# Performance work log

Hardware: AMD Instinct MI355X
Metric: run time of the kernel (lower is better)

The kernel has to match this reference:

```python
import jax, jax.numpy as jnp
import numpy as np

N = 4096

def setup_inputs() -> dict:
    key = jax.random.key(0)
    kA, kB = jax.random.split(key)
    A = jnp.tril(jax.random.normal(kA, (N, N), dtype=jnp.float32))
    B = jnp.tril(jax.random.normal(kB, (N, N), dtype=jnp.float32))
    return {"A": A, "B": B}

def reference(A, B):
    # Product of two lower-triangular matrices; result is lower-triangular.
    # tril applied to the dense matmul reproduces the intended math exactly
    # (and zeroes any numerical noise in the structural-zero upper triangle).
    return jnp.tril(jnp.matmul(A, B))
```

## Files before the change

kernel.cpp:

```cpp
#include <hip/hip_runtime.h>
#include <stdint.h>

#define NN 4096
#define NB 32
#define BK 32

#define NHEAVY 136
#define NHUNITS 272
#define NLIGHT 392
#define ZBASE 664
#define TGRID 1160

#define PGRID 8328

typedef __bf16 bf16x8 __attribute__((ext_vector_type(8)));
typedef float f32x4 __attribute__((ext_vector_type(4)));
typedef unsigned short ushort8 __attribute__((ext_vector_type(8)));

__device__ __forceinline__ unsigned short f2bf(float x) {
    union { float f; unsigned int u; } v; v.f = x;
    unsigned int u = v.u;
    u += 0x7fffu + ((u >> 16) & 1u);
    return (unsigned short)(u >> 16);
}

#define GLOAD16(g, l) __builtin_amdgcn_global_load_lds( \
    (const __attribute__((address_space(1))) unsigned int*)(g), \
    (__attribute__((address_space(3))) unsigned int*)(l), 16, 0, 0)

__device__ __forceinline__ void heavy_map(int h, int& bi, int& bj) {
    int t = h, d = NB - 1;
    while (t >= NB - d) { t -= NB - d; --d; }
    bj = t; bi = t + d;
}

__global__ __launch_bounds__(256) void prep(const float* __restrict__ A,
                                            const float* __restrict__ B,
                                            unsigned short* __restrict__ Ab,
                                            unsigned short* __restrict__ Bt,
                                            float* __restrict__ C) {
    __shared__ float tile[64][65];
    int bid = blockIdx.x;
    int tid = threadIdx.x;

    if (bid < 4096) {
        int i = bid;
        int nslots = (((i >> 7) + 1) * 128) >> 3;
        const float4* src = reinterpret_cast<const float4*>(A + (size_t)i * NN);
        unsigned short* dst = Ab + (size_t)i * NN;
        for (int p = tid; p < nslots; p += 256) {
            float4 x0 = src[p * 2], x1 = src[p * 2 + 1];
            ushort8 o;
            o[0] = f2bf(x0.x); o[1] = f2bf(x0.y); o[2] = f2bf(x0.z); o[3] = f2bf(x0.w);
            o[4] = f2bf(x1.x); o[5] = f2bf(x1.y); o[6] = f2bf(x1.z); o[7] = f2bf(x1.w);
            *reinterpret_cast<ushort8*>(dst + p * 8) = o;
        }
        return;
    }
    if (bid < 8192) {
        int s = bid - 4096;
        int n64 = s >> 6, k64 = s & 63;
        if (k64 < (n64 & ~1)) return;
        int n0 = n64 * 64, k0 = k64 * 64;
        int tx = tid & 63, ty = tid >> 6;
#pragma unroll
        for (int r = 0; r < 16; ++r) {
            int k = ty + r * 4;
            tile[k][tx] = B[(size_t)(k0 + k) * NN + n0 + tx];
        }
        __syncthreads();
#pragma unroll
        for (int r = 0; r < 16; ++r) {
            int n = ty + r * 4;
            Bt[(size_t)(n0 + n) * NN + k0 + tx] = f2bf(tile[tx][n]);
        }
        return;
    }
    int h = bid - 8192;
    int bi, bj; heavy_map(h, bi, bj);
    float4 z = make_float4(0.f, 0.f, 0.f, 0.f);
    float4* cp = reinterpret_cast<float4*>(C + (size_t)bi * 128 * NN + (size_t)bj * 128);
#pragma unroll
    for (int i2 = 0; i2 < 16; ++i2) {
        int slot = tid + i2 * 256;
        int row = slot >> 5, c4 = slot & 31;
        cp[(size_t)row * (NN / 4) + c4] = z;
    }
}

__global__ __launch_bounds__(256) void trimm(const unsigned short* __restrict__ Ab,
                                             const unsigned short* __restrict__ Bt,
                                             float* __restrict__ C) {
    int bid = blockIdx.x;
    int tid = threadIdx.x;
    int lane = tid & 63;
    int w = tid >> 6;

    int bi, bj;
    bool heavy = false;
    int k_lo, k_hi;

    if (bid >= ZBASE) {
        int t = bid - ZBASE;
        int r = 0, cnt = NB - 1;
        while (t >= cnt) { t -= cnt; ++r; --cnt; }
        bi = r; bj = r + 1 + t;
        float4 z = make_float4(0.f, 0.f, 0.f, 0.f);
        float4* cp = reinterpret_cast<float4*>(C + (size_t)bi * 128 * NN + (size_t)bj * 128);
#pragma unroll
        for (int i2 = 0; i2 < 16; ++i2) {
            int slot = tid + i2 * 256;
            int row = slot >> 5, c4 = slot & 31;
            cp[(size_t)row * (NN / 4) + c4] = z;
        }
        return;
    }
    if (bid < NHUNITS) {
        heavy = true;
        int h = bid >> 1, half = bid & 1;
        heavy_map(h, bi, bj);
        k_lo = bj * 128;
        k_hi = (bi + 1) * 128;
        int len = (k_hi - k_lo) >> 1;
        if (half == 0) k_hi = k_lo + len;
        else           k_lo = k_lo + len;
    } else {
        int t = bid - NHUNITS, d = 15;
        while (t >= NB - d) { t -= NB - d; --d; }
        bj = t; bi = t + d;
        k_lo = bj * 128;
        k_hi = (bi + 1) * 128;
    }

    __shared__ unsigned short As[128 * BK];
    __shared__ unsigned short Bs[128 * BK];

    int wr = w >> 1, wc = w & 1;

    int srow = w * 32 + (lane >> 2);
    int skoff = (lane & 3) * 8;
    const unsigned short* gA0 = Ab + (size_t)(bi * 128 + srow) * NN + skoff;
    const unsigned short* gA1 = gA0 + (size_t)16 * NN;
    const unsigned short* gB0 = Bt + (size_t)(bj * 128 + srow) * NN + skoff;
    const unsigned short* gB1 = gB0 + (size_t)16 * NN;
    unsigned short* lA0 = As + w * 1024;
    unsigned short* lA1 = lA0 + 512;
    unsigned short* lB0 = Bs + w * 1024;
    unsigned short* lB1 = lB0 + 512;

    f32x4 acc[4][4];
#pragma unroll
    for (int mi = 0; mi < 4; ++mi)
#pragma unroll
        for (int ni = 0; ni < 4; ++ni)
            acc[mi][ni] = (f32x4){0.f, 0.f, 0.f, 0.f};

    int arow = wr * 64 + (lane & 15);
    int brow = wc * 64 + (lane & 15);
    int kq = (lane >> 4) * 8;

    for (int kt = k_lo; kt < k_hi; kt += BK) {
        GLOAD16(gA0 + kt, lA0);
        GLOAD16(gA1 + kt, lA1);
        GLOAD16(gB0 + kt, lB0);
        GLOAD16(gB1 + kt, lB1);
        __syncthreads();

        bf16x8 af[4], bfr[4];
#pragma unroll
        for (int mi = 0; mi < 4; ++mi)
            af[mi] = *reinterpret_cast<const bf16x8*>(&As[(arow + mi * 16) * BK + kq]);
#pragma unroll
        for (int ni = 0; ni < 4; ++ni)
            bfr[ni] = *reinterpret_cast<const bf16x8*>(&Bs[(brow + ni * 16) * BK + kq]);
#pragma unroll
        for (int mi = 0; mi < 4; ++mi)
#pragma unroll
            for (int ni = 0; ni < 4; ++ni)
                acc[mi][ni] = __builtin_amdgcn_mfma_f32_16x16x32_bf16(af[mi], bfr[ni], acc[mi][ni], 0, 0, 0);
        __syncthreads();
    }

    int crow0 = bi * 128 + wr * 64 + (lane >> 4) * 4;
    int ccol0 = bj * 128 + wc * 64 + (lane & 15);
    if (heavy) {
#pragma unroll
        for (int mi = 0; mi < 4; ++mi)
#pragma unroll
            for (int ni = 0; ni < 4; ++ni) {
                float* cp = C + (size_t)(crow0 + mi * 16) * NN + ccol0 + ni * 16;
#pragma unroll
                for (int r2 = 0; r2 < 4; ++r2)
                    atomicAdd(&cp[(size_t)r2 * NN], acc[mi][ni][r2]);
            }
    } else {
#pragma unroll
        for (int mi = 0; mi < 4; ++mi)
#pragma unroll
            for (int ni = 0; ni < 4; ++ni) {
                float* cp = C + (size_t)(crow0 + mi * 16) * NN + ccol0 + ni * 16;
#pragma unroll
                for (int r2 = 0; r2 < 4; ++r2)
                    cp[(size_t)r2 * NN] = acc[mi][ni][r2];
            }
    }
}

extern "C" void kernel_launch(void* const* d_in, const int* in_sizes, int n_in,
                              void* d_out, int out_size, void* d_ws, size_t ws_size,
                              hipStream_t stream) {
    const float* A = (const float*)d_in[0];
    const float* B = (const float*)d_in[1];
    float* C = (float*)d_out;
    unsigned short* Ab = (unsigned short*)d_ws;
    unsigned short* Bt = Ab + (size_t)NN * NN;
    prep<<<PGRID, 256, 0, stream>>>(A, B, Ab, Bt, C);
    trimm<<<TGRID, 256, 0, stream>>>(Ab, Bt, C);
}
```

Baseline: 90.19 us.

## Double-buffer LDS tiles to prefetch the next K-slice during MFMA compute

Splits the A and B shared-memory tiles into two buffers. The first K-slice is loaded before the loop, and each iteration issues the global-to-LDS loads for the next slice right after the barrier, then computes on the current buffer. This drops the second barrier per iteration and hides global load latency behind the MFMA work. In exchange, LDS use per block doubles, which may reduce how many blocks fit on each compute unit.

```diff
diff --git a/kernel.cpp b/kernel.cpp
--- a/kernel.cpp
+++ b/kernel.cpp
@@ -7,7 +7,6 @@
 
 #define NHEAVY 136
 #define NHUNITS 272
-#define NLIGHT 392
 #define ZBASE 664
 #define TGRID 1160
 
@@ -132,8 +131,8 @@
         k_hi = (bi + 1) * 128;
     }
 
-    __shared__ unsigned short As[128 * BK];
-    __shared__ unsigned short Bs[128 * BK];
+    __shared__ unsigned short As[2][128 * BK];
+    __shared__ unsigned short Bs[2][128 * BK];
 
     int wr = w >> 1, wc = w & 1;
 
@@ -143,10 +142,6 @@
     const unsigned short* gA1 = gA0 + (size_t)16 * NN;
     const unsigned short* gB0 = Bt + (size_t)(bj * 128 + srow) * NN + skoff;
     const unsigned short* gB1 = gB0 + (size_t)16 * NN;
-    unsigned short* lA0 = As + w * 1024;
-    unsigned short* lA1 = lA0 + 512;
-    unsigned short* lB0 = Bs + w * 1024;
-    unsigned short* lB1 = lB0 + 512;
 
     f32x4 acc[4][4];
 #pragma unroll
@@ -159,26 +154,42 @@
     int brow = wc * 64 + (lane & 15);
     int kq = (lane >> 4) * 8;
 
+    {
+        unsigned short* a = &As[0][w * 1024];
+        unsigned short* b = &Bs[0][w * 1024];
+        GLOAD16(gA0 + k_lo, a);
+        GLOAD16(gA1 + k_lo, a + 512);
+        GLOAD16(gB0 + k_lo, b);
+        GLOAD16(gB1 + k_lo, b + 512);
+    }
+    int cur = 0;
+
     for (int kt = k_lo; kt < k_hi; kt += BK) {
-        GLOAD16(gA0 + kt, lA0);
-        GLOAD16(gA1 + kt, lA1);
-        GLOAD16(gB0 + kt, lB0);
-        GLOAD16(gB1 + kt, lB1);
         __syncthreads();
 
+        if (kt + BK < k_hi) {
+            unsigned short* a = &As[cur ^ 1][w * 1024];
+            unsigned short* b = &Bs[cur ^ 1][w * 1024];
+            GLOAD16(gA0 + kt + BK, a);
+            GLOAD16(gA1 + kt + BK, a + 512);
+            GLOAD16(gB0 + kt + BK, b);
+            GLOAD16(gB1 + kt + BK, b + 512);
+        }
+
         bf16x8 af[4], bfr[4];
 #pragma unroll
         for (int mi = 0; mi < 4; ++mi)
-            af[mi] = *reinterpret_cast<const bf16x8*>(&As[(arow + mi * 16) * BK + kq]);
+            af[mi] = *reinterpret_cast<const bf16x8*>(&As[cur][(arow + mi * 16) * BK + kq]);
 #pragma unroll
         for (int ni = 0; ni < 4; ++ni)
-            bfr[ni] = *reinterpret_cast<const bf16x8*>(&Bs[(brow + ni * 16) * BK + kq]);
+            bfr[ni] = *reinterpret_cast<const bf16x8*>(&Bs[cur][(brow + ni * 16) * BK + kq]);
 #pragma unroll
         for (int mi = 0; mi < 4; ++mi)
 #pragma unroll
             for (int ni = 0; ni < 4; ++ni)
                 acc[mi][ni] = __builtin_amdgcn_mfma_f32_16x16x32_bf16(af[mi], bfr[ni], acc[mi][ni], 0, 0, 0);
-        __syncthreads();
+
+        cur ^= 1;
     }
 
     int crow0 = bi * 128 + wr * 64 + (lane >> 4) * 4;
```

Result: faster. 85.86 us (-4.8%).
